# Kernel optimization log

Measured on AMD Instinct MI355X. Metric: run time of the kernel, lower is better.

The kernel has to match this reference:

```python
import jax, jax.numpy as jnp
import numpy as np

N_NODES = 100000
N_ADJ = 11
E = 1600000
D_IN = 128
D_OUT = 16
C = 1.0
MIN_NORM = 1e-15
PROJ_EPS = 4e-3  # float32 eps used by HGCN PoincareBall.proj


def _norm(x):
    return jnp.maximum(jnp.linalg.norm(x, axis=-1, keepdims=True), MIN_NORM)


def _artanh(x):
    return jnp.arctanh(jnp.clip(x, -1.0 + 1e-7, 1.0 - 1e-7))


def logmap0(x, c):
    sqrt_c = c ** 0.5
    xn = _norm(x)
    return x / xn / sqrt_c * _artanh(sqrt_c * xn)


def expmap0(u, c):
    sqrt_c = c ** 0.5
    un = _norm(u)
    return jnp.tanh(sqrt_c * un) * u / (sqrt_c * un)


def proj(x, c):
    xn = _norm(x)
    maxnorm = (1.0 - PROJ_EPS) / (c ** 0.5)
    return jnp.where(xn > maxnorm, x / xn * maxnorm, x)


def setup_inputs() -> dict:
    key = jax.random.key(0)
    k1, k2, k3, k4, k5, k6 = jax.random.split(key, 6)
    # points inside the Poincare ball (||x|| << 1)
    x = jax.random.normal(k1, (N_NODES, D_IN), dtype=jnp.float32) * 0.01
    adj_rows = jax.random.randint(k2, (N_ADJ, E), 0, N_NODES, dtype=jnp.int32)
    adj_cols = jax.random.randint(k3, (N_ADJ, E), 0, N_NODES, dtype=jnp.int32)
    adj_vals = jax.random.uniform(k4, (N_ADJ, E), dtype=jnp.float32) * (1.0 / 16.0)
    fan_in = D_IN
    bound = float(np.sqrt(6.0 / fan_in))  # kaiming_uniform-ish scale
    adj_weight = jax.random.uniform(k5, (N_ADJ, D_IN, D_OUT), dtype=jnp.float32,
                                    minval=-bound, maxval=bound)
    bias = jax.random.normal(k6, (D_OUT,), dtype=jnp.float32) * 0.01
    return {"x": x, "adj_rows": adj_rows, "adj_cols": adj_cols,
            "adj_vals": adj_vals, "adj_weight": adj_weight, "bias": bias}


def reference(x, adj_rows, adj_cols, adj_vals, adj_weight, bias):
    n = x.shape[0]
    x_tangent = logmap0(x, C)                      # [N, D_IN]
    acc = jnp.zeros((n, D_OUT), dtype=x.dtype)
    for i in range(N_ADJ):                          # fixed small relation loop
        support_t = x_tangent @ adj_weight[i]       # [N, 16]
        gathered = support_t[adj_cols[i]] * adj_vals[i][:, None]  # [E, 16]
        agg = jax.ops.segment_sum(gathered, adj_rows[i], num_segments=n)
        acc = acc + proj(expmap0(agg, C), C)
    return acc / 11.0 + bias
```

## Files before the change

### kernel.cpp

```cpp
#include <hip/hip_runtime.h>
#include <math.h>

#define NN 100000
#define NADJ 11
#define EE 1600000
#define DI 128
#define DO 16
#define SMAX 64

static constexpr float MIN_NORM = 1e-15f;
static constexpr float MAXNORM  = 1.0f - 4e-3f;

__global__ void k_scale(const float* __restrict__ x, float* __restrict__ scale) {
    int lane   = threadIdx.x & 63;
    int wid    = (blockIdx.x * blockDim.x + threadIdx.x) >> 6;
    int nwav   = (gridDim.x * blockDim.x) >> 6;
    for (int n = wid; n < NN; n += nwav) {
        float2 v = ((const float2*)(x + (size_t)n * DI))[lane];
        float ss = v.x * v.x + v.y * v.y;
        #pragma unroll
        for (int off = 1; off < 64; off <<= 1) ss += __shfl_xor(ss, off);
        if (lane == 0) {
            float xn = fmaxf(sqrtf(ss), MIN_NORM);
            float xc = fminf(xn, 1.0f - 1e-7f);
            scale[n] = atanhf(xc) / xn;
        }
    }
}

template<int G>
__global__ __launch_bounds__(256) void k_gemm(const float* __restrict__ x,
                                              const float* __restrict__ scale,
                                              const float* __restrict__ W,
                                              float* __restrict__ support) {
    constexpr int COLS = 16 * G;
    __shared__ float xs[64][36];
    __shared__ float ws[COLS][36];
    const int t  = threadIdx.x;
    const int tc = t & 15;
    const int tr = t >> 4;
    const int n0 = blockIdx.x * 64;

    float acc[4][G];
    #pragma unroll
    for (int m = 0; m < 4; ++m)
        #pragma unroll
        for (int j = 0; j < G; ++j) acc[m][j] = 0.f;

    for (int kb = 0; kb < 4; ++kb) {
        __syncthreads();
        for (int idx = t; idx < 64 * 8; idx += 256) {
            int r = idx >> 3, k4 = idx & 7;
            int n = n0 + r;
            float4 v = make_float4(0.f, 0.f, 0.f, 0.f);
            if (n < NN) v = ((const float4*)(x + (size_t)n * DI + kb * 32))[k4];
            *(float4*)&xs[r][k4 * 4] = v;
        }
        for (int idx = t; idx < G * 32 * 4; idx += 256) {
            int j = idx >> 7, rem = idx & 127, kk = rem >> 2, o4 = rem & 3;
            float4 v = *(const float4*)(W + ((size_t)j * DI + kb * 32 + kk) * DO + o4 * 4);
            ws[j * 16 + o4 * 4 + 0][kk] = v.x;
            ws[j * 16 + o4 * 4 + 1][kk] = v.y;
            ws[j * 16 + o4 * 4 + 2][kk] = v.z;
            ws[j * 16 + o4 * 4 + 3][kk] = v.w;
        }
        __syncthreads();
        #pragma unroll
        for (int kk4 = 0; kk4 < 8; ++kk4) {
            float4 xv[4];
            #pragma unroll
            for (int m = 0; m < 4; ++m) xv[m] = *(const float4*)&xs[tr * 4 + m][kk4 * 4];
            #pragma unroll
            for (int j = 0; j < G; ++j) {
                float4 wv = *(const float4*)&ws[j * 16 + tc][kk4 * 4];
                #pragma unroll
                for (int m = 0; m < 4; ++m)
                    acc[m][j] += xv[m].x * wv.x + xv[m].y * wv.y
                               + xv[m].z * wv.z + xv[m].w * wv.w;
            }
        }
    }
    #pragma unroll
    for (int m = 0; m < 4; ++m) {
        int n = n0 + tr * 4 + m;
        if (n < NN) {
            float s = scale[n];
            #pragma unroll
            for (int j = 0; j < G; ++j)
                support[((size_t)j * NN + n) * DO + tc] = acc[m][j] * s;
        }
    }
}

__global__ __launch_bounds__(256) void k_place(const int* __restrict__ rows,
                                               const int* __restrict__ cols,
                                               const float* __restrict__ vals,
                                               int* __restrict__ cursor,
                                               float2* __restrict__ packed,
                                               int nrel) {
    unsigned total  = (unsigned)nrel * EE;
    unsigned stride = gridDim.x * blockDim.x;
    for (unsigned g = blockIdx.x * blockDim.x + threadIdx.x; g < total; g += stride) {
        unsigned ro = g / EE;
        int row = rows[g];
        int pos = atomicAdd(&cursor[ro * NN + row], 1);
        if (pos < SMAX)
            packed[((size_t)ro * NN + row) * SMAX + pos] =
                make_float2(vals[g], __int_as_float(cols[g]));
    }
}

__global__ __launch_bounds__(256) void k_gather(const int* __restrict__ cursor,
                                                const float2* __restrict__ packed,
                                                const float* __restrict__ support,
                                                float* __restrict__ out,
                                                int r0, int nrel) {
    int lane = threadIdx.x & 15;
    int n = (blockIdx.x * blockDim.x + threadIdx.x) >> 4;
    if (n >= NN) return;
    float oacc = 0.f;
    for (int ro = 0; ro < nrel; ++ro) {
        int cnt = cursor[ro * NN + n];
        if (cnt > SMAX) cnt = SMAX;
        const float2* seg = packed + ((size_t)ro * NN + n) * SMAX;
        const float*  sup = support + (size_t)(r0 + ro) * NN * DO;
        float acc = 0.f;
        for (int j = 0; j < cnt; ++j) {
            float2 ec = seg[j];
            acc += ec.x * sup[(size_t)__float_as_int(ec.y) * DO + lane];
        }
        float ss = acc * acc;
        ss += __shfl_xor(ss, 1, 16);
        ss += __shfl_xor(ss, 2, 16);
        ss += __shfl_xor(ss, 4, 16);
        ss += __shfl_xor(ss, 8, 16);
        float un = fmaxf(sqrtf(ss), MIN_NORM);
        float th = tanhf(un);
        float rn = fmaxf(th, MIN_NORM);
        float sc = (rn > MAXNORM) ? (MAXNORM / rn) : 1.0f;
        oacc += acc * (th / un) * sc;
    }
    out[(size_t)n * DO + lane] += oacc * (1.0f / 11.0f);
}

__global__ void k_init_out(const float* __restrict__ bias, float* __restrict__ out) {
    int idx = blockIdx.x * blockDim.x + threadIdx.x;
    if (idx < NN * 16) out[idx] = bias[idx & 15];
}

extern "C" void kernel_launch(void* const* d_in, const int* in_sizes, int n_in,
                              void* d_out, int out_size, void* d_ws, size_t ws_size,
                              hipStream_t stream) {
    const float* x        = (const float*)d_in[0];
    const int*   adj_rows = (const int*)d_in[1];
    const int*   adj_cols = (const int*)d_in[2];
    const float* adj_vals = (const float*)d_in[3];
    const float* adj_w    = (const float*)d_in[4];
    const float* bias     = (const float*)d_in[5];
    float*       out      = (float*)d_out;

    char* p = (char*)d_ws;
    auto alloc = [&](size_t bytes) {
        char* r = p;
        p += (bytes + 255) & ~(size_t)255;
        return r;
    };
    float* scale   = (float*)alloc((size_t)NN * 4);
    float* support = (float*)alloc((size_t)NADJ * NN * DO * 4);

    size_t used    = (size_t)(p - (char*)d_ws);
    size_t per_rel = ((size_t)NN * 4 + 256) + ((size_t)NN * SMAX * 8 + 256);
    size_t avail   = (ws_size > used) ? ws_size - used : 0;
    int c = (int)(avail / per_rel);
    if (c < 1) c = 1;
    if (c > NADJ) c = NADJ;
    int*    cursor = (int*)alloc((size_t)c * NN * 4);
    float2* packed = (float2*)alloc((size_t)c * NN * SMAX * 8);

    k_scale<<<512, 256, 0, stream>>>(x, scale);
    k_init_out<<<(NN * 16 + 255) / 256, 256, 0, stream>>>(bias, out);
    k_gemm<NADJ><<<(NN + 63) / 64, 256, 0, stream>>>(x, scale, adj_w, support);

    for (int r0 = 0; r0 < NADJ; r0 += c) {
        int nr = (NADJ - r0 < c) ? (NADJ - r0) : c;
        hipMemsetAsync(cursor, 0, (size_t)nr * NN * 4, stream);
        k_place<<<2048, 256, 0, stream>>>(adj_rows + (size_t)r0 * EE,
                                          adj_cols + (size_t)r0 * EE,
                                          adj_vals + (size_t)r0 * EE,
                                          cursor, packed, nr);
        k_gather<<<(NN * 16 + 255) / 256, 256, 0, stream>>>(cursor, packed, support,
                                                            out, r0, nr);
    }
}
```

Before: 1.916 ms.

## Replace per-row edge slots with 256-row bins and shared-memory aggregation

Edges are no longer scattered into fixed 64-slot segments per destination row via global atomics. Each block first buffers them in shared memory per 256-row bin and flushes them in chunks to bin segments. A per-bin kernel then accumulates into a shared-memory tile with LDS atomics and writes the aggregates, and a separate final kernel applies expmap/proj. The GEMM output is also staged through shared memory to get coalesced float4 stores. This targets the scattered global atomics and the wasteful, uncoalesced 64-slot writes, at the cost of an extra aggregate buffer pass and a fixed per-bin capacity (4608) that could silently drop edges if a bin overflows.

Result: slower. 5.078 ms (+165.0%).

```diff
diff --git a/kernel.cpp b/kernel.cpp
--- a/kernel.cpp
+++ b/kernel.cpp
@@ -6,7 +6,10 @@
 #define EE 1600000
 #define DI 128
 #define DO 16
-#define SMAX 64
+
+#define NBINS 391
+#define BCAP 16
+#define SEGCAP 4608
 
 static constexpr float MIN_NORM = 1e-15f;
 static constexpr float MAXNORM  = 1.0f - 4e-3f;
@@ -29,10 +32,10 @@
 }
 
 template<int G>
-__global__ __launch_bounds__(256) void k_gemm(const float* __restrict__ x,
-                                              const float* __restrict__ scale,
-                                              const float* __restrict__ W,
-                                              float* __restrict__ support) {
+__global__ __launch_bounds__(256, 4) void k_gemm(const float* __restrict__ x,
+                                                 const float* __restrict__ scale,
+                                                 const float* __restrict__ W,
+                                                 float* __restrict__ support) {
     constexpr int COLS = 16 * G;
     __shared__ float xs[64][36];
     __shared__ float ws[COLS][36];
@@ -80,56 +83,153 @@
             }
         }
     }
+    float sv[4];
     #pragma unroll
     for (int m = 0; m < 4; ++m) {
         int n = n0 + tr * 4 + m;
+        sv[m] = (n < NN) ? scale[n] : 0.f;
+    }
+    float* st = &xs[0][0];
+    const int row = t >> 2, q = t & 3;
+    for (int j = 0; j < G; ++j) {
+        __syncthreads();
+        #pragma unroll
+        for (int m = 0; m < 4; ++m)
+            st[(tr * 4 + m) * 17 + tc] = acc[m][j] * sv[m];
+        __syncthreads();
+        int n = n0 + row;
         if (n < NN) {
-            float s = scale[n];
-            #pragma unroll
-            for (int j = 0; j < G; ++j)
-                support[((size_t)j * NN + n) * DO + tc] = acc[m][j] * s;
-        }
-    }
-}
-
-__global__ __launch_bounds__(256) void k_place(const int* __restrict__ rows,
-                                               const int* __restrict__ cols,
-                                               const float* __restrict__ vals,
-                                               int* __restrict__ cursor,
-                                               float2* __restrict__ packed,
-                                               int nrel) {
-    unsigned total  = (unsigned)nrel * EE;
-    unsigned stride = gridDim.x * blockDim.x;
-    for (unsigned g = blockIdx.x * blockDim.x + threadIdx.x; g < total; g += stride) {
-        unsigned ro = g / EE;
-        int row = rows[g];
-        int pos = atomicAdd(&cursor[ro * NN + row], 1);
-        if (pos < SMAX)
-            packed[((size_t)ro * NN + row) * SMAX + pos] =
-                make_float2(vals[g], __int_as_float(cols[g]));
-    }
-}
-
-__global__ __launch_bounds__(256) void k_gather(const int* __restrict__ cursor,
-                                                const float2* __restrict__ packed,
-                                                const float* __restrict__ support,
-                                                float* __restrict__ out,
-                                                int r0, int nrel) {
-    int lane = threadIdx.x & 15;
-    int n = (blockIdx.x * blockDim.x + threadIdx.x) >> 4;
+            float4 v = make_float4(st[row * 17 + q * 4 + 0], st[row * 17 + q * 4 + 1],
+                                   st[row * 17 + q * 4 + 2], st[row * 17 + q * 4 + 3]);
+            *(float4*)&support[((size_t)j * NN + n) * DO + q * 4] = v;
+        }
+    }
+}
+
+__global__ __launch_bounds__(256) void k_bin(const int* __restrict__ rows,
+                                             const int* __restrict__ cols,
+                                             const float* __restrict__ vals,
+                                             int* __restrict__ gcur,
+                                             float2* __restrict__ packed) {
+    __shared__ int    cnt[NBINS];
+    __shared__ float2 buf[NBINS][BCAP];
+    __shared__ int    fl_b[256];
+    __shared__ int    fl_gp[256];
+    __shared__ int    nflush;
+
+    const int t  = threadIdx.x;
+    const int ro = blockIdx.y;
+    const size_t ebase = (size_t)ro * EE;
+    int*    cur = gcur + (size_t)ro * NBINS;
+    float2* pk  = packed + (size_t)ro * NBINS * SEGCAP;
+
+    const int nper = (EE + gridDim.x - 1) / gridDim.x;
+    const int e0 = blockIdx.x * nper;
+    const int e1 = (e0 + nper < EE) ? e0 + nper : EE;
+
+    for (int b = t; b < NBINS; b += 256) cnt[b] = 0;
+    __syncthreads();
+
+    for (int eb = e0; eb < e1; eb += 256) {
+        int e = eb + t;
+        if (e < e1) {
+            int   r = rows[ebase + e];
+            int   c = cols[ebase + e];
+            float v = vals[ebase + e];
+            int bin = r >> 8;
+            float2 entry = make_float2(v, __uint_as_float(((unsigned)(r & 255) << 17) | (unsigned)c));
+            int pos = atomicAdd(&cnt[bin], 1);
+            if (pos < BCAP) {
+                buf[bin][pos] = entry;
+            } else {
+                int gp = atomicAdd(&cur[bin], 1);
+                if (gp < SEGCAP) pk[(size_t)bin * SEGCAP + gp] = entry;
+            }
+        }
+        __syncthreads();
+        if (t == 0) nflush = 0;
+        __syncthreads();
+        for (int b = t; b < NBINS; b += 256) {
+            int c = cnt[b];
+            if (c >= BCAP) {
+                int i = atomicAdd(&nflush, 1);
+                fl_b[i]  = b;
+                fl_gp[i] = atomicAdd(&cur[b], BCAP);
+                cnt[b] = 0;
+            }
+        }
+        __syncthreads();
+        int nf = nflush, o = t & 15;
+        for (int j = t >> 4; j < nf; j += 16) {
+            int b = fl_b[j];
+            int gp = fl_gp[j] + o;
+            if (gp < SEGCAP) pk[(size_t)b * SEGCAP + gp] = buf[b][o];
+        }
+        __syncthreads();
+    }
+    int o = t & 15;
+    for (int b = t >> 4; b < NBINS; b += 16) {
+        int c = cnt[b];
+        int gp0 = 0;
+        if (o == 0 && c > 0) gp0 = atomicAdd(&cur[b], c);
+        gp0 = __shfl(gp0, (threadIdx.x & 63) & ~15);
+        if (o < c) {
+            int gp = gp0 + o;
+            if (gp < SEGCAP) pk[(size_t)b * SEGCAP + gp] = buf[b][o];
+        }
+    }
+}
+
+__global__ __launch_bounds__(256) void k_agg(const int* __restrict__ gcur,
+                                             const float2* __restrict__ packed,
+                                             const float* __restrict__ support,
+                                             float* __restrict__ agg, int r0) {
+    __shared__ float acc[256 * 17];
+    const int t   = threadIdx.x;
+    const int bin = blockIdx.x;
+    const int ro  = blockIdx.y;
+
+    for (int i = t; i < 256 * 17; i += 256) acc[i] = 0.f;
+    __syncthreads();
+
+    int c = gcur[(size_t)ro * NBINS + bin];
+    if (c > SEGCAP) c = SEGCAP;
+    const float2* seg = packed + ((size_t)ro * NBINS + bin) * SEGCAP;
+    const float*  sup = support + (size_t)(r0 + ro) * NN * DO;
+
+    const int o = t & 15;
+    for (int i = t >> 4; i < c; i += 16) {
+        float2 e = seg[i];
+        unsigned p = __float_as_uint(e.y);
+        int col = (int)(p & 0x1FFFFu);
+        int r8  = (int)(p >> 17);
+        atomicAdd(&acc[r8 * 17 + o], e.x * sup[(size_t)col * DO + o]);
+    }
+    __syncthreads();
+
+    const int n0 = bin * 256;
+    const int row0 = t >> 2, q = t & 3;
+    #pragma unroll
+    for (int pass = 0; pass < 4; ++pass) {
+        int row = pass * 64 + row0;
+        int n = n0 + row;
+        if (n < NN) {
+            float4 v = make_float4(acc[row * 17 + q * 4 + 0], acc[row * 17 + q * 4 + 1],
+                                   acc[row * 17 + q * 4 + 2], acc[row * 17 + q * 4 + 3]);
+            *(float4*)&agg[((size_t)ro * NN + n) * DO + q * 4] = v;
+        }
+    }
+}
+
+__global__ __launch_bounds__(256) void k_final(const float* __restrict__ agg,
+                                               float* __restrict__ out, int nrel) {
+    int t = blockIdx.x * blockDim.x + threadIdx.x;
+    int n = t >> 4, o = t & 15;
     if (n >= NN) return;
-    float oacc = 0.f;
+    float oa = 0.f;
     for (int ro = 0; ro < nrel; ++ro) {
-        int cnt = cursor[ro * NN + n];
-        if (cnt > SMAX) cnt = SMAX;
-        const float2* seg = packed + ((size_t)ro * NN + n) * SMAX;
-        const float*  sup = support + (size_t)(r0 + ro) * NN * DO;
-        float acc = 0.f;
-        for (int j = 0; j < cnt; ++j) {
-            float2 ec = seg[j];
-            acc += ec.x * sup[(size_t)__float_as_int(ec.y) * DO + lane];
-        }
-        float ss = acc * acc;
+        float u = agg[((size_t)ro * NN + n) * DO + o];
+        float ss = u * u;
         ss += __shfl_xor(ss, 1, 16);
         ss += __shfl_xor(ss, 2, 16);
         ss += __shfl_xor(ss, 4, 16);
@@ -138,9 +238,9 @@
         float th = tanhf(un);
         float rn = fmaxf(th, MIN_NORM);
         float sc = (rn > MAXNORM) ? (MAXNORM / rn) : 1.0f;
-        oacc += acc * (th / un) * sc;
-    }
-    out[(size_t)n * DO + lane] += oacc * (1.0f / 11.0f);
+        oa += u * (th / un) * sc;
+    }
+    out[(size_t)n * DO + o] += oa * (1.0f / 11.0f);
 }
 
 __global__ void k_init_out(const float* __restrict__ bias, float* __restrict__ out) {
@@ -169,26 +269,29 @@
     float* support = (float*)alloc((size_t)NADJ * NN * DO * 4);
 
     size_t used    = (size_t)(p - (char*)d_ws);
-    size_t per_rel = ((size_t)NN * 4 + 256) + ((size_t)NN * SMAX * 8 + 256);
+    size_t per_rel = ((size_t)NBINS * 4 + 256)
+                   + ((size_t)NBINS * SEGCAP * 8 + 256)
+                   + ((size_t)NN * DO * 4 + 256);
     size_t avail   = (ws_size > used) ? ws_size - used : 0;
-    int c = (int)(avail / per_rel);
-    if (c < 1) c = 1;
-    if (c > NADJ) c = NADJ;
-    int*    cursor = (int*)alloc((size_t)c * NN * 4);
-    float2* packed = (float2*)alloc((size_t)c * NN * SMAX * 8);
+    int cr = (int)(avail / per_rel);
+    if (cr < 1) cr = 1;
+    if (cr > NADJ) cr = NADJ;
+    int*    gcur   = (int*)alloc((size_t)cr * NBINS * 4);
+    float2* packed = (float2*)alloc((size_t)cr * NBINS * SEGCAP * 8);
+    float*  agg    = (float*)alloc((size_t)cr * NN * DO * 4);
 
     k_scale<<<512, 256, 0, stream>>>(x, scale);
     k_init_out<<<(NN * 16 + 255) / 256, 256, 0, stream>>>(bias, out);
     k_gemm<NADJ><<<(NN + 63) / 64, 256, 0, stream>>>(x, scale, adj_w, support);
 
-    for (int r0 = 0; r0 < NADJ; r0 += c) {
-        int nr = (NADJ - r0 < c) ? (NADJ - r0) : c;
-        hipMemsetAsync(cursor, 0, (size_t)nr * NN * 4, stream);
-        k_place<<<2048, 256, 0, stream>>>(adj_rows + (size_t)r0 * EE,
-                                          adj_cols + (size_t)r0 * EE,
-                                          adj_vals + (size_t)r0 * EE,
-                                          cursor, packed, nr);
-        k_gather<<<(NN * 16 + 255) / 256, 256, 0, stream>>>(cursor, packed, support,
-                                                            out, r0, nr);
-    }
-}
+    for (int r0 = 0; r0 < NADJ; r0 += cr) {
+        int nr = (NADJ - r0 < cr) ? (NADJ - r0) : cr;
+        hipMemsetAsync(gcur, 0, (size_t)nr * NBINS * 4, stream);
+        k_bin<<<dim3(192, nr), 256, 0, stream>>>(adj_rows + (size_t)r0 * EE,
+                                                 adj_cols + (size_t)r0 * EE,
+                                                 adj_vals + (size_t)r0 * EE,
+                                                 gcur, packed);
+        k_agg<<<dim3(NBINS, nr), 256, 0, stream>>>(gcur, packed, support, agg, r0);
+        k_final<<<(NN * 16 + 255) / 256, 256, 0, stream>>>(agg, out, nr);
+    }
+}
```
